# Performance work log

Hardware: AMD Instinct MI355X
Metric: run time of the kernel (lower is better)

Reference implementation:

```python
import jax, jax.numpy as jnp
import numpy as np

D = 1  # dilation


def _unfold3x3(x, d):
    # x: [B, C, H, W] -> [B, H*W, 9, C]; matches torch.nn.Unfold(kernel_size=3,
    # dilation=d, padding=d, stride=1) followed by the module's reshapes.
    B, C, H, W = x.shape
    xp = jnp.pad(x, ((0, 0), (0, 0), (d, d), (d, d)))
    pats = [xp[:, :, i * d:i * d + H, j * d:j * d + W] for i in range(3) for j in range(3)]
    p = jnp.stack(pats, axis=0)  # [9, B, C, H, W], kernel positions row-major (center = 4)
    return p.transpose(1, 3, 4, 0, 2).reshape(B, H * W, 9, C)


def _masked_bn(h, m, gamma, beta, eps=1e-5):
    # BatchNorm1d in training mode applied only to rows selected by bool mask m
    # (the torch code gathers rows, BNs them, scatters back into zeros).
    # Stats are the biased mean/var over the selected rows, per channel.
    axes = tuple(range(h.ndim - 1))
    mf = m[..., None].astype(h.dtype)
    n = jnp.maximum(mf.sum(), 1.0)
    mean = (h * mf).sum(axes) / n
    var = (((h - mean) ** 2 * mf)).sum(axes) / n
    return (h - mean) * jax.lax.rsqrt(var + eps) * gamma + beta


def setup_inputs() -> dict:
    key = jax.random.key(0)
    ks = jax.random.split(key, 8)
    B, H, W = 2, 64, 1024
    Cin, Cout, Cm = 64, 64, 4
    s = 0.1
    x = jax.random.normal(ks[0], (B, Cm + Cin, H, W), jnp.float32)
    mask = (jax.random.uniform(ks[1], (B, 1, H, W)) > 0.3).astype(jnp.float32)
    return {
        "x": x,
        "mask": mask,
        "w1": jax.random.normal(ks[2], (8, Cm), jnp.float32) * s,
        "bn1_g": jnp.ones(8, jnp.float32),
        "bn1_b": jnp.zeros(8, jnp.float32),
        "w2": jax.random.normal(ks[3], (1, 8), jnp.float32) * s,
        "b2": jnp.zeros(1, jnp.float32),
        "g1": jax.random.normal(ks[4], (8, Cm), jnp.float32) * s,
        "gbn1_g": jnp.ones(8, jnp.float32),
        "gbn1_b": jnp.zeros(8, jnp.float32),
        "g2": jax.random.normal(ks[5], (8, 8), jnp.float32) * s,
        "gbn2_g": jnp.ones(8, jnp.float32),
        "gbn2_b": jnp.zeros(8, jnp.float32),
        "w_agg": jax.random.normal(ks[6], (Cout, 72 + Cin), jnp.float32) * s,
        "abn_g": jnp.ones(Cout, jnp.float32),
        "abn_b": jnp.zeros(Cout, jnp.float32),
    }


def reference(x, mask, w1, bn1_g, bn1_b, w2, b2, g1, gbn1_g, gbn1_b, g2, gbn2_g, gbn2_b, w_agg, abn_g, abn_b):
    B, C, H, W = x.shape
    xu = _unfold3x3(x, D)                      # [B, HW, 9, C]
    mu = _unfold3x3(mask, D)[..., 0]           # [B, HW, 9]
    msel = mu > 0                              # valid-neighbor mask
    mp0 = msel[:, :, 4]                        # valid-center mask [B, HW]
    pn = xu[..., :4] - xu[:, :, 4:5, :4]       # relative meta coords [B, HW, 9, 4]
    feats = xu[..., 4:]                        # neighbor features [B, HW, 9, Cin]

    # weight branch (dense compute + mask == torch's gather/scatter)
    h = _masked_bn(pn @ w1.T, msel, bn1_g, bn1_b)
    h = jax.nn.relu(h) @ w2.T + b2             # [B, HW, 9, 1]
    wts = jnp.where(msel, h[..., 0], 0.0)      # zeros at invalid neighbors pre-softmax
    wts = jax.nn.softmax(wts, axis=-1)[..., None]

    fagg = (wts * feats).sum(axis=2)           # [B, HW, Cin]

    # geo branch
    g = jax.nn.relu(_masked_bn(pn @ g1.T, msel, gbn1_g, gbn1_b))
    g = jax.nn.relu(_masked_bn(g @ g2.T, msel, gbn2_g, gbn2_b))
    g = jnp.where(msel[..., None], g, 0.0)
    g = (wts * g).reshape(B, H * W, 72)

    # aggregation over valid centers
    out = jnp.concatenate([fagg, g], axis=-1) @ w_agg.T
    out = jax.nn.relu(_masked_bn(out, mp0, abn_g, abn_b))
    out = jnp.where(mp0[..., None], out, 0.0)  # [B, HW, Cout]
    return out.transpose(0, 2, 1).reshape(B, -1, H, W)  # fold with k=1 == reshape
```

## Files before the change

### kernel.cpp

```cpp
#include <hip/hip_runtime.h>

#define HW_ 65536
#define W_ 1024
#define H_ 64
#define B_ 2
#define C_ 68
#define NPIX 131072
#define EPS 1e-5f

typedef __attribute__((ext_vector_type(8))) short short8;
typedef __attribute__((ext_vector_type(4))) float floatx4;

__device__ __forceinline__ unsigned short f2bf(float f) {
  unsigned u = __float_as_uint(f);
  u += 0x7fffu + ((u >> 16) & 1u);
  return (unsigned short)(u >> 16);
}
__device__ __forceinline__ unsigned pack2(float a, float b) {
  return (unsigned)f2bf(a) | ((unsigned)f2bf(b) << 16);
}
__device__ __forceinline__ float wred(float v) {
  v += __shfl_xor(v, 1);  v += __shfl_xor(v, 2);  v += __shfl_xor(v, 4);
  v += __shfl_xor(v, 8);  v += __shfl_xor(v, 16); v += __shfl_xor(v, 32);
  return v;
}
__device__ __forceinline__ int swz_tile(int bid) {
  return (bid & 7) * 64 + (bid >> 3);
}

__global__ __launch_bounds__(256) void k_stats1(
    const float* __restrict__ x, const float* __restrict__ mask,
    const float* __restrict__ w1, const float* __restrict__ g1,
    float* __restrict__ ws) {
  int half = blockIdx.x >> 9;
  int p = swz_tile(blockIdx.x & 511) * 256 + threadIdx.x;
  int b = p >> 16, s = p & (HW_ - 1);
  int h = s >> 10, w = s & (W_ - 1);
  const float* xb = x + (size_t)b * C_ * HW_;
  const float* mb = mask + (size_t)b * HW_;
  float xc0 = xb[s], xc1 = xb[HW_ + s], xc2 = xb[2 * HW_ + s], xc3 = xb[3 * HW_ + s];

  float acc[34];
#pragma unroll
  for (int i = 0; i < 34; i++) acc[i] = 0.f;
  if (half == 0) acc[33] = (mb[s] > 0.f) ? 1.f : 0.f;

#pragma unroll
  for (int k = 0; k < 9; k++) {
    bool mine = (k < 5) ? (half == 0) : (half == 1);
    if (!mine) continue;
    int di = k / 3 - 1, dj = k % 3 - 1;
    int hh = h + di, ww = w + dj;
    bool inb = ((unsigned)hh < (unsigned)H_) && ((unsigned)ww < (unsigned)W_);
    int ns = hh * W_ + ww;
    float mval = inb ? mb[ns] : 0.f;
    if (mval > 0.f) {
      float pn0 = xb[ns] - xc0;
      float pn1 = xb[HW_ + ns] - xc1;
      float pn2 = xb[2 * HW_ + ns] - xc2;
      float pn3 = xb[3 * HW_ + ns] - xc3;
      acc[32] += 1.f;
#pragma unroll
      for (int o = 0; o < 8; o++) {
        float ta = pn0 * w1[o * 4] + pn1 * w1[o * 4 + 1] + pn2 * w1[o * 4 + 2] + pn3 * w1[o * 4 + 3];
        acc[o] += ta; acc[8 + o] += ta * ta;
        float tg = pn0 * g1[o * 4] + pn1 * g1[o * 4 + 1] + pn2 * g1[o * 4 + 2] + pn3 * g1[o * 4 + 3];
        acc[16 + o] += tg; acc[24 + o] += tg * tg;
      }
    }
  }
  __shared__ float red[4][34];
  int lane = threadIdx.x & 63, wave = threadIdx.x >> 6;
#pragma unroll
  for (int i = 0; i < 34; i++) {
    float rv = wred(acc[i]);
    if (lane == 0) red[wave][i] = rv;
  }
  __syncthreads();
  if (threadIdx.x < 34)
    atomicAdd(&ws[threadIdx.x],
              red[0][threadIdx.x] + red[1][threadIdx.x] + red[2][threadIdx.x] + red[3][threadIdx.x]);
}

__global__ __launch_bounds__(256) void k_stats2(
    const float* __restrict__ x, const float* __restrict__ mask,
    const float* __restrict__ g1, const float* __restrict__ gbn1_g,
    const float* __restrict__ gbn1_b, const float* __restrict__ g2,
    float* __restrict__ ws) {
  __shared__ float sc[8], sh[8];
  if (threadIdx.x < 8) {
    int o = threadIdx.x;
    float n = fmaxf(ws[32], 1.f);
    float mean = ws[16 + o] / n;
    float var = ws[24 + o] / n - mean * mean;
    float s_ = gbn1_g[o] * rsqrtf(var + EPS);
    sc[o] = s_; sh[o] = gbn1_b[o] - mean * s_;
  }
  __syncthreads();

  int half = blockIdx.x >> 9;
  int p = swz_tile(blockIdx.x & 511) * 256 + threadIdx.x;
  int b = p >> 16, s = p & (HW_ - 1);
  int h = s >> 10, w = s & (W_ - 1);
  const float* xb = x + (size_t)b * C_ * HW_;
  const float* mb = mask + (size_t)b * HW_;
  float xc0 = xb[s], xc1 = xb[HW_ + s], xc2 = xb[2 * HW_ + s], xc3 = xb[3 * HW_ + s];

  float acc2[16];
#pragma unroll
  for (int i = 0; i < 16; i++) acc2[i] = 0.f;

#pragma unroll
  for (int k = 0; k < 9; k++) {
    bool mine = (k < 5) ? (half == 0) : (half == 1);
    if (!mine) continue;
    int di = k / 3 - 1, dj = k % 3 - 1;
    int hh = h + di, ww = w + dj;
    bool inb = ((unsigned)hh < (unsigned)H_) && ((unsigned)ww < (unsigned)W_);
    int ns = hh * W_ + ww;
    float mval = inb ? mb[ns] : 0.f;
    if (mval > 0.f) {
      float pn0 = xb[ns] - xc0;
      float pn1 = xb[HW_ + ns] - xc1;
      float pn2 = xb[2 * HW_ + ns] - xc2;
      float pn3 = xb[3 * HW_ + ns] - xc3;
      float gb[8];
#pragma unroll
      for (int o = 0; o < 8; o++) {
        float tg = pn0 * g1[o * 4] + pn1 * g1[o * 4 + 1] + pn2 * g1[o * 4 + 2] + pn3 * g1[o * 4 + 3];
        gb[o] = fmaxf(sc[o] * tg + sh[o], 0.f);
      }
#pragma unroll
      for (int j = 0; j < 8; j++) {
        float t2 = 0.f;
#pragma unroll
        for (int o = 0; o < 8; o++) t2 += gb[o] * g2[j * 8 + o];
        acc2[j] += t2; acc2[8 + j] += t2 * t2;
      }
    }
  }
  __shared__ float red[4][16];
  int lane = threadIdx.x & 63, wave = threadIdx.x >> 6;
#pragma unroll
  for (int i = 0; i < 16; i++) {
    float rv = wred(acc2[i]);
    if (lane == 0) red[wave][i] = rv;
  }
  __syncthreads();
  if (threadIdx.x < 16)
    atomicAdd(&ws[40 + threadIdx.x],
              red[0][threadIdx.x] + red[1][threadIdx.x] + red[2][threadIdx.x] + red[3][threadIdx.x]);
}

__global__ __launch_bounds__(512, 4) void k_fused(
    const float* __restrict__ x, const float* __restrict__ mask,
    const float* __restrict__ w1, const float* __restrict__ bn1_g,
    const float* __restrict__ bn1_b, const float* __restrict__ w2,
    const float* __restrict__ b2, const float* __restrict__ g1,
    const float* __restrict__ gbn1_g, const float* __restrict__ gbn1_b,
    const float* __restrict__ g2, const float* __restrict__ gbn2_g,
    const float* __restrict__ gbn2_b, const float* __restrict__ w_agg,
    const float* __restrict__ ws, float* __restrict__ out_pre,
    float* __restrict__ wsum) {
  __shared__ uint4 vecA[17][256];
  __shared__ float evb[9][256];
  __shared__ float sA[8], hA[8], sG1[8], hG1[8], sG2[8], hG2[8];

  if (threadIdx.x < 24) {
    int o = threadIdx.x & 7;
    float n = fmaxf(ws[32], 1.f);
    float sum, sum2, gma, bta;
    if (threadIdx.x < 8)       { sum = ws[o];      sum2 = ws[8 + o];  gma = bn1_g[o];  bta = bn1_b[o]; }
    else if (threadIdx.x < 16) { sum = ws[16 + o]; sum2 = ws[24 + o]; gma = gbn1_g[o]; bta = gbn1_b[o]; }
    else                       { sum = ws[40 + o]; sum2 = ws[48 + o]; gma = gbn2_g[o]; bta = gbn2_b[o]; }
    float mean = sum / n, var = sum2 / n - mean * mean;
    float s_ = gma * rsqrtf(var + EPS);
    float sft = bta - mean * s_;
    if (threadIdx.x < 8)       { sA[o] = s_;  hA[o] = sft; }
    else if (threadIdx.x < 16) { sG1[o] = s_; hG1[o] = sft; }
    else                       { sG2[o] = s_; hG2[o] = sft; }
  }
  __syncthreads();

  int tid = threadIdx.x;
  int half = tid >> 8;
  int pix = tid & 255;
  int tile = swz_tile(blockIdx.x);
  int p0 = tile * 256;
  int p = p0 + pix;
  int b = p >> 16, s = p & (HW_ - 1);
  int h = s >> 10, w = s & (W_ - 1);
  const float* xb = x + (size_t)b * C_ * HW_;
  const float* mb = mask + (size_t)b * HW_;
  float xc0 = xb[s], xc1 = xb[HW_ + s], xc2 = xb[2 * HW_ + s], xc3 = xb[3 * HW_ + s];
  float b2v = b2[0];

  unsigned mbits = 0u;
#pragma unroll
  for (int k = 0; k < 9; k++) {
    bool mine = (k < 5) ? (half == 0) : (half == 1);
    if (!mine) continue;
    int di = k / 3 - 1, dj = k % 3 - 1;
    int hh = h + di, ww = w + dj;
    bool inb = ((unsigned)hh < (unsigned)H_) && ((unsigned)ww < (unsigned)W_);
    int ns = hh * W_ + ww;
    float mval = inb ? mb[ns] : 0.f;
    float wp = 0.f;
    if (mval > 0.f) {
      mbits |= (1u << k);
      float pn0 = xb[ns] - xc0;
      float pn1 = xb[HW_ + ns] - xc1;
      float pn2 = xb[2 * HW_ + ns] - xc2;
      float pn3 = xb[3 * HW_ + ns] - xc3;
      float accw = 0.f;
#pragma unroll
      for (int o = 0; o < 8; o++) {
        float ta = pn0 * w1[o * 4] + pn1 * w1[o * 4 + 1] + pn2 * w1[o * 4 + 2] + pn3 * w1[o * 4 + 3];
        accw += fmaxf(sA[o] * ta + hA[o], 0.f) * w2[o];
      }
      wp = accw + b2v;
    }
    evb[k][pix] = wp;
  }
  __syncthreads();

  float ev[9];
  float mx = -1e30f;
#pragma unroll
  for (int k = 0; k < 9; k++) { ev[k] = evb[k][pix]; mx = fmaxf(mx, ev[k]); }
  float den = 0.f;
#pragma unroll
  for (int k = 0; k < 9; k++) { ev[k] = __expf(ev[k] - mx); den += ev[k]; }
  float inv = 1.f / den;

#pragma unroll
  for (int k = 0; k < 9; k++) {
    bool mine = (k < 5) ? (half == 0) : (half == 1);
    if (!mine) continue;
    uint4 pk; pk.x = pk.y = pk.z = pk.w = 0u;
    if ((mbits >> k) & 1u) {
      int di = k / 3 - 1, dj = k % 3 - 1;
      int ns = (h + di) * W_ + (w + dj);
      float wt = ev[k] * inv;
      float pn0 = xb[ns] - xc0;
      float pn1 = xb[HW_ + ns] - xc1;
      float pn2 = xb[2 * HW_ + ns] - xc2;
      float pn3 = xb[3 * HW_ + ns] - xc3;
      float gb[8];
#pragma unroll
      for (int o = 0; o < 8; o++) {
        float tg = pn0 * g1[o * 4] + pn1 * g1[o * 4 + 1] + pn2 * g1[o * 4 + 2] + pn3 * g1[o * 4 + 3];
        gb[o] = fmaxf(sG1[o] * tg + hG1[o], 0.f);
      }
      float gv[8];
#pragma unroll
      for (int j = 0; j < 8; j++) {
        float t2 = 0.f;
#pragma unroll
        for (int o = 0; o < 8; o++) t2 += gb[o] * g2[j * 8 + o];
        float gg = fmaxf(sG2[j] * t2 + hG2[j], 0.f);
        gv[j] = wt * gg;
      }
      pk.x = pack2(gv[0], gv[1]); pk.y = pack2(gv[2], gv[3]);
      pk.z = pack2(gv[4], gv[5]); pk.w = pack2(gv[6], gv[7]);
    }
    vecA[8 + k][pix] = pk;
  }

  float facc[32];
#pragma unroll
  for (int c = 0; c < 32; c++) facc[c] = 0.f;
#pragma unroll
  for (int k = 0; k < 9; k++) {
    int di = k / 3 - 1, dj = k % 3 - 1;
    int hh = h + di, ww = w + dj;
    bool inb = ((unsigned)hh < (unsigned)H_) && ((unsigned)ww < (unsigned)W_);
    if (inb) {
      int ns = hh * W_ + ww;
      float wt = ev[k] * inv;
      const float* xf = xb + (size_t)(4 + half * 32) * HW_ + ns;
#pragma unroll
      for (int c = 0; c < 32; c++) facc[c] += wt * xf[c * HW_];
    }
  }
#pragma unroll
  for (int c0 = 0; c0 < 32; c0 += 8) {
    uint4 pk;
    pk.x = pack2(facc[c0], facc[c0 + 1]);     pk.y = pack2(facc[c0 + 2], facc[c0 + 3]);
    pk.z = pack2(facc[c0 + 4], facc[c0 + 5]); pk.w = pack2(facc[c0 + 6], facc[c0 + 7]);
    vecA[(half * 32 + c0) >> 3][pix] = pk;
  }
  __syncthreads();

  int lane = tid & 63, wave = tid >> 6;
  int q = lane >> 4, r = lane & 15;
  int wr = wave >> 1, wc = wave & 1;

  short8 Bf[2][5];
#pragma unroll
  for (int nt = 0; nt < 2; nt++) {
    int n = wc * 32 + nt * 16 + r;
#pragma unroll
    for (int ks = 0; ks < 5; ks++) {
      int k0 = ks * 32 + q * 8;
      uint4 pk; pk.x = pk.y = pk.z = pk.w = 0u;
      if (k0 < 136) {
        float4 f0 = *reinterpret_cast<const float4*>(w_agg + n * 136 + k0);
        float4 f1 = *reinterpret_cast<const float4*>(w_agg + n * 136 + k0 + 4);
        pk.x = pack2(f0.x, f0.y); pk.y = pack2(f0.z, f0.w);
        pk.z = pack2(f1.x, f1.y); pk.w = pack2(f1.z, f1.w);
      }
      Bf[nt][ks] = *reinterpret_cast<short8*>(&pk);
    }
  }

  floatx4 acc[4][2];
#pragma unroll
  for (int m = 0; m < 4; m++)
#pragma unroll
    for (int nt = 0; nt < 2; nt++) acc[m][nt] = (floatx4){0.f, 0.f, 0.f, 0.f};

#pragma unroll
  for (int m = 0; m < 4; m++) {
    int pixm = (wr * 4 + m) * 16 + r;
    short8 Af[5];
#pragma unroll
    for (int ks = 0; ks < 5; ks++) {
      int chunk = ks * 4 + q;
      if (chunk < 17)
        Af[ks] = *reinterpret_cast<const short8*>(&vecA[chunk][pixm]);
      else
        Af[ks] = (short8){0, 0, 0, 0, 0, 0, 0, 0};
    }
#pragma unroll
    for (int nt = 0; nt < 2; nt++)
#pragma unroll
      for (int ks = 0; ks < 5; ks++)
        acc[m][nt] = __builtin_amdgcn_mfma_f32_16x16x32_bf16(Af[ks], Bf[nt][ks], acc[m][nt], 0, 0, 0);
  }

  float aS[2] = {0.f, 0.f}, aQ[2] = {0.f, 0.f};
  int s0 = p0 & (HW_ - 1);
#pragma unroll
  for (int m = 0; m < 4; m++) {
    int mt = wr * 4 + m;
    int srow = s0 + mt * 16 + q * 4;
    float4 mv = *reinterpret_cast<const float4*>(mb + srow);
    float m0 = (mv.x > 0.f) ? 1.f : 0.f, m1 = (mv.y > 0.f) ? 1.f : 0.f;
    float m2 = (mv.z > 0.f) ? 1.f : 0.f, m3 = (mv.w > 0.f) ? 1.f : 0.f;
#pragma unroll
    for (int nt = 0; nt < 2; nt++) {
      int ch = wc * 32 + nt * 16 + r;
      float4 ov;
      ov.x = acc[m][nt][0]; ov.y = acc[m][nt][1];
      ov.z = acc[m][nt][2]; ov.w = acc[m][nt][3];
      aS[nt] += ov.x * m0 + ov.y * m1 + ov.z * m2 + ov.w * m3;
      aQ[nt] += ov.x * ov.x * m0 + ov.y * ov.y * m1 + ov.z * ov.z * m2 + ov.w * ov.w * m3;
      *reinterpret_cast<float4*>(out_pre + ((size_t)(b * 64 + ch)) * HW_ + srow) = ov;
    }
  }

  __syncthreads();
  float* rS = (float*)&vecA[0][0];
  float* rQ = rS + 256;
#pragma unroll
  for (int nt = 0; nt < 2; nt++) {
    float v1 = aS[nt], v2 = aQ[nt];
    v1 += __shfl_xor(v1, 16); v1 += __shfl_xor(v1, 32);
    v2 += __shfl_xor(v2, 16); v2 += __shfl_xor(v2, 32);
    if (lane < 16) { rS[wave * 32 + nt * 16 + lane] = v1; rQ[wave * 32 + nt * 16 + lane] = v2; }
  }
  __syncthreads();
  if (tid < 64) {
    int c = tid;
    int wc_ = c >> 5, nt_ = (c >> 4) & 1, r_ = c & 15;
    float s1 = 0.f, s2 = 0.f;
#pragma unroll
    for (int wr_ = 0; wr_ < 4; wr_++) {
      int idx = (wr_ * 2 + wc_) * 32 + nt_ * 16 + r_;
      s1 += rS[idx]; s2 += rQ[idx];
    }
    atomicAdd(&wsum[64 + c], s1);
    atomicAdd(&wsum[128 + c], s2);
  }
}

__global__ __launch_bounds__(256) void k_final(
    const float* __restrict__ out_pre, const float* __restrict__ mask,
    const float* __restrict__ abn_g, const float* __restrict__ abn_b,
    const float* __restrict__ ws, float* __restrict__ out) {
  __shared__ float sc[64], sh[64];
  if (threadIdx.x < 64) {
    int c = threadIdx.x;
    float n0 = fmaxf(ws[33], 1.f);
    float mean = ws[64 + c] / n0;
    float var = ws[128 + c] / n0 - mean * mean;
    float s_ = abn_g[c] * rsqrtf(var + EPS);
    sc[c] = s_; sh[c] = abn_b[c] - mean * s_;
  }
  __syncthreads();
  int i4 = (blockIdx.x * 256 + threadIdx.x) * 4;
  if (i4 >= B_ * 64 * HW_) return;
  int c = (i4 >> 16) & 63;
  int b = i4 >> 22;
  int s = i4 & (HW_ - 1);
  float4 v = *reinterpret_cast<const float4*>(out_pre + i4);
  float4 m = *reinterpret_cast<const float4*>(mask + (size_t)b * HW_ + s);
  float4 o;
  o.x = (m.x > 0.f) ? fmaxf(v.x * sc[c] + sh[c], 0.f) : 0.f;
  o.y = (m.y > 0.f) ? fmaxf(v.y * sc[c] + sh[c], 0.f) : 0.f;
  o.z = (m.z > 0.f) ? fmaxf(v.z * sc[c] + sh[c], 0.f) : 0.f;
  o.w = (m.w > 0.f) ? fmaxf(v.w * sc[c] + sh[c], 0.f) : 0.f;
  *reinterpret_cast<float4*>(out + i4) = o;
}

extern "C" void kernel_launch(void* const* d_in, const int* in_sizes, int n_in,
                              void* d_out, int out_size, void* d_ws, size_t ws_size,
                              hipStream_t stream) {
  const float* x      = (const float*)d_in[0];
  const float* mask   = (const float*)d_in[1];
  const float* w1     = (const float*)d_in[2];
  const float* bn1_g  = (const float*)d_in[3];
  const float* bn1_b  = (const float*)d_in[4];
  const float* w2     = (const float*)d_in[5];
  const float* b2     = (const float*)d_in[6];
  const float* g1     = (const float*)d_in[7];
  const float* gbn1_g = (const float*)d_in[8];
  const float* gbn1_b = (const float*)d_in[9];
  const float* g2     = (const float*)d_in[10];
  const float* gbn2_g = (const float*)d_in[11];
  const float* gbn2_b = (const float*)d_in[12];
  const float* w_agg  = (const float*)d_in[13];
  const float* abn_g  = (const float*)d_in[14];
  const float* abn_b  = (const float*)d_in[15];
  float* out = (float*)d_out;

  size_t need = 1024 + (size_t)NPIX * 64 * 4;
  if (ws_size < need) return;

  float* wsf = (float*)d_ws;
  float* out_pre = (float*)((char*)d_ws + 1024);

  hipMemsetAsync(d_ws, 0, 1024, stream);
  k_stats1<<<1024, 256, 0, stream>>>(x, mask, w1, g1, wsf);
  k_stats2<<<1024, 256, 0, stream>>>(x, mask, g1, gbn1_g, gbn1_b, g2, wsf);
  k_fused<<<512, 512, 0, stream>>>(x, mask, w1, bn1_g, bn1_b, w2, b2, g1,
                                   gbn1_g, gbn1_b, g2, gbn2_g, gbn2_b, w_agg,
                                   wsf, out_pre, wsf);
  k_final<<<8192, 256, 0, stream>>>(out_pre, mask, abn_g, abn_b, wsf, out);
}
```

Measured before the change: 208.2 us.

## Fuse final BN into main kernel via grid barrier, split stats into quarters

Removes the out_pre intermediate buffer and the separate k_final kernel. k_fused now keeps its accumulators in registers, waits at a software grid-wide barrier until all blocks have added their channel statistics, and then applies BN, ReLU and the mask before writing the output directly. This saves a 32MB write and read of the intermediate. Separately, the stats kernels split the 9 neighbors across 4 block groups instead of 2, launching 2048 blocks for more parallelism. The barrier relies on all 512 blocks being co-resident and has a spin timeout that could silently give wrong results if they are not.

```diff
diff --git a/kernel.cpp b/kernel.cpp
--- a/kernel.cpp
+++ b/kernel.cpp
@@ -6,6 +6,7 @@
 #define B_ 2
 #define C_ 68
 #define NPIX 131072
+#define NBLK_F 512
 #define EPS 1e-5f
 
 typedef __attribute__((ext_vector_type(8))) short short8;
@@ -27,12 +28,44 @@
 __device__ __forceinline__ int swz_tile(int bid) {
   return (bid & 7) * 64 + (bid >> 3);
 }
+__device__ __forceinline__ float wsld(const float* p) {
+  return __hip_atomic_load(p, __ATOMIC_RELAXED, __HIP_MEMORY_SCOPE_AGENT);
+}
+
+__device__ __forceinline__ void gridbar(unsigned* bar, unsigned nblk) {
+  __syncthreads();
+  if (threadIdx.x == 0) {
+    __threadfence();
+    unsigned gen = __hip_atomic_load(&bar[1], __ATOMIC_RELAXED, __HIP_MEMORY_SCOPE_AGENT);
+    unsigned arrived =
+        __hip_atomic_fetch_add(&bar[0], 1u, __ATOMIC_ACQ_REL, __HIP_MEMORY_SCOPE_AGENT);
+    if (arrived == nblk - 1) {
+      __hip_atomic_store(&bar[0], 0u, __ATOMIC_RELAXED, __HIP_MEMORY_SCOPE_AGENT);
+      __hip_atomic_store(&bar[1], gen + 1u, __ATOMIC_RELEASE, __HIP_MEMORY_SCOPE_AGENT);
+    } else {
+      long long spins = 0;
+      while (__hip_atomic_load(&bar[1], __ATOMIC_ACQUIRE, __HIP_MEMORY_SCOPE_AGENT) == gen) {
+        if (++spins > (1LL << 22)) break;
+        __builtin_amdgcn_s_sleep(8);
+      }
+    }
+    __threadfence();
+  }
+  __syncthreads();
+}
+
+__device__ __forceinline__ bool owns_k(int quarter, int k) {
+  return (quarter == 0) ? (k < 3)
+       : (quarter == 1) ? (k >= 3 && k < 5)
+       : (quarter == 2) ? (k >= 5 && k < 7)
+       :                  (k >= 7);
+}
 
 __global__ __launch_bounds__(256) void k_stats1(
     const float* __restrict__ x, const float* __restrict__ mask,
     const float* __restrict__ w1, const float* __restrict__ g1,
     float* __restrict__ ws) {
-  int half = blockIdx.x >> 9;
+  int quarter = blockIdx.x >> 9;
   int p = swz_tile(blockIdx.x & 511) * 256 + threadIdx.x;
   int b = p >> 16, s = p & (HW_ - 1);
   int h = s >> 10, w = s & (W_ - 1);
@@ -43,12 +76,11 @@
   float acc[34];
 #pragma unroll
   for (int i = 0; i < 34; i++) acc[i] = 0.f;
-  if (half == 0) acc[33] = (mb[s] > 0.f) ? 1.f : 0.f;
+  if (quarter == 1) acc[33] = (mb[s] > 0.f) ? 1.f : 0.f;
 
 #pragma unroll
   for (int k = 0; k < 9; k++) {
-    bool mine = (k < 5) ? (half == 0) : (half == 1);
-    if (!mine) continue;
+    if (!owns_k(quarter, k)) continue;
     int di = k / 3 - 1, dj = k % 3 - 1;
     int hh = h + di, ww = w + dj;
     bool inb = ((unsigned)hh < (unsigned)H_) && ((unsigned)ww < (unsigned)W_);
@@ -98,7 +130,7 @@
   }
   __syncthreads();
 
-  int half = blockIdx.x >> 9;
+  int quarter = blockIdx.x >> 9;
   int p = swz_tile(blockIdx.x & 511) * 256 + threadIdx.x;
   int b = p >> 16, s = p & (HW_ - 1);
   int h = s >> 10, w = s & (W_ - 1);
@@ -112,8 +144,7 @@
 
 #pragma unroll
   for (int k = 0; k < 9; k++) {
-    bool mine = (k < 5) ? (half == 0) : (half == 1);
-    if (!mine) continue;
+    if (!owns_k(quarter, k)) continue;
     int di = k / 3 - 1, dj = k % 3 - 1;
     int hh = h + di, ww = w + dj;
     bool inb = ((unsigned)hh < (unsigned)H_) && ((unsigned)ww < (unsigned)W_);
@@ -160,11 +191,13 @@
     const float* __restrict__ gbn1_g, const float* __restrict__ gbn1_b,
     const float* __restrict__ g2, const float* __restrict__ gbn2_g,
     const float* __restrict__ gbn2_b, const float* __restrict__ w_agg,
-    const float* __restrict__ ws, float* __restrict__ out_pre,
-    float* __restrict__ wsum) {
+    const float* __restrict__ abn_g, const float* __restrict__ abn_b,
+    float* __restrict__ ws, float* __restrict__ out) {
+  unsigned* bar = (unsigned*)(ws + 248);
   __shared__ uint4 vecA[17][256];
   __shared__ float evb[9][256];
   __shared__ float sA[8], hA[8], sG1[8], hG1[8], sG2[8], hG2[8];
+  __shared__ float scD[64], shD[64];
 
   if (threadIdx.x < 24) {
     int o = threadIdx.x & 7;
@@ -350,13 +383,9 @@
     float m2 = (mv.z > 0.f) ? 1.f : 0.f, m3 = (mv.w > 0.f) ? 1.f : 0.f;
 #pragma unroll
     for (int nt = 0; nt < 2; nt++) {
-      int ch = wc * 32 + nt * 16 + r;
-      float4 ov;
-      ov.x = acc[m][nt][0]; ov.y = acc[m][nt][1];
-      ov.z = acc[m][nt][2]; ov.w = acc[m][nt][3];
-      aS[nt] += ov.x * m0 + ov.y * m1 + ov.z * m2 + ov.w * m3;
-      aQ[nt] += ov.x * ov.x * m0 + ov.y * ov.y * m1 + ov.z * ov.z * m2 + ov.w * ov.w * m3;
-      *reinterpret_cast<float4*>(out_pre + ((size_t)(b * 64 + ch)) * HW_ + srow) = ov;
+      aS[nt] += acc[m][nt][0] * m0 + acc[m][nt][1] * m1 + acc[m][nt][2] * m2 + acc[m][nt][3] * m3;
+      aQ[nt] += acc[m][nt][0] * acc[m][nt][0] * m0 + acc[m][nt][1] * acc[m][nt][1] * m1 +
+                acc[m][nt][2] * acc[m][nt][2] * m2 + acc[m][nt][3] * acc[m][nt][3] * m3;
     }
   }
 
@@ -380,38 +409,38 @@
       int idx = (wr_ * 2 + wc_) * 32 + nt_ * 16 + r_;
       s1 += rS[idx]; s2 += rQ[idx];
     }
-    atomicAdd(&wsum[64 + c], s1);
-    atomicAdd(&wsum[128 + c], s2);
-  }
-}
-
-__global__ __launch_bounds__(256) void k_final(
-    const float* __restrict__ out_pre, const float* __restrict__ mask,
-    const float* __restrict__ abn_g, const float* __restrict__ abn_b,
-    const float* __restrict__ ws, float* __restrict__ out) {
-  __shared__ float sc[64], sh[64];
-  if (threadIdx.x < 64) {
-    int c = threadIdx.x;
-    float n0 = fmaxf(ws[33], 1.f);
-    float mean = ws[64 + c] / n0;
-    float var = ws[128 + c] / n0 - mean * mean;
+    atomicAdd(&ws[64 + c], s1);
+    atomicAdd(&ws[128 + c], s2);
+  }
+
+  gridbar(bar, NBLK_F);
+
+  if (tid < 64) {
+    int c = tid;
+    float n0 = fmaxf(wsld(&ws[33]), 1.f);
+    float mean = wsld(&ws[64 + c]) / n0;
+    float var = wsld(&ws[128 + c]) / n0 - mean * mean;
     float s_ = abn_g[c] * rsqrtf(var + EPS);
-    sc[c] = s_; sh[c] = abn_b[c] - mean * s_;
-  }
-  __syncthreads();
-  int i4 = (blockIdx.x * 256 + threadIdx.x) * 4;
-  if (i4 >= B_ * 64 * HW_) return;
-  int c = (i4 >> 16) & 63;
-  int b = i4 >> 22;
-  int s = i4 & (HW_ - 1);
-  float4 v = *reinterpret_cast<const float4*>(out_pre + i4);
-  float4 m = *reinterpret_cast<const float4*>(mask + (size_t)b * HW_ + s);
-  float4 o;
-  o.x = (m.x > 0.f) ? fmaxf(v.x * sc[c] + sh[c], 0.f) : 0.f;
-  o.y = (m.y > 0.f) ? fmaxf(v.y * sc[c] + sh[c], 0.f) : 0.f;
-  o.z = (m.z > 0.f) ? fmaxf(v.z * sc[c] + sh[c], 0.f) : 0.f;
-  o.w = (m.w > 0.f) ? fmaxf(v.w * sc[c] + sh[c], 0.f) : 0.f;
-  *reinterpret_cast<float4*>(out + i4) = o;
+    scD[c] = s_; shD[c] = abn_b[c] - mean * s_;
+  }
+  __syncthreads();
+#pragma unroll
+  for (int m = 0; m < 4; m++) {
+    int mt = wr * 4 + m;
+    int srow = s0 + mt * 16 + q * 4;
+    float4 mv = *reinterpret_cast<const float4*>(mb + srow);
+#pragma unroll
+    for (int nt = 0; nt < 2; nt++) {
+      int ch = wc * 32 + nt * 16 + r;
+      float sc_ = scD[ch], sh_ = shD[ch];
+      float4 ov;
+      ov.x = (mv.x > 0.f) ? fmaxf(acc[m][nt][0] * sc_ + sh_, 0.f) : 0.f;
+      ov.y = (mv.y > 0.f) ? fmaxf(acc[m][nt][1] * sc_ + sh_, 0.f) : 0.f;
+      ov.z = (mv.z > 0.f) ? fmaxf(acc[m][nt][2] * sc_ + sh_, 0.f) : 0.f;
+      ov.w = (mv.w > 0.f) ? fmaxf(acc[m][nt][3] * sc_ + sh_, 0.f) : 0.f;
+      *reinterpret_cast<float4*>(out + ((size_t)(b * 64 + ch)) * HW_ + srow) = ov;
+    }
+  }
 }
 
 extern "C" void kernel_launch(void* const* d_in, const int* in_sizes, int n_in,
@@ -435,17 +464,13 @@
   const float* abn_b  = (const float*)d_in[15];
   float* out = (float*)d_out;
 
-  size_t need = 1024 + (size_t)NPIX * 64 * 4;
-  if (ws_size < need) return;
-
+  if (ws_size < 1024) return;
   float* wsf = (float*)d_ws;
-  float* out_pre = (float*)((char*)d_ws + 1024);
 
   hipMemsetAsync(d_ws, 0, 1024, stream);
-  k_stats1<<<1024, 256, 0, stream>>>(x, mask, w1, g1, wsf);
-  k_stats2<<<1024, 256, 0, stream>>>(x, mask, g1, gbn1_g, gbn1_b, g2, wsf);
-  k_fused<<<512, 512, 0, stream>>>(x, mask, w1, bn1_g, bn1_b, w2, b2, g1,
-                                   gbn1_g, gbn1_b, g2, gbn2_g, gbn2_b, w_agg,
-                                   wsf, out_pre, wsf);
-  k_final<<<8192, 256, 0, stream>>>(out_pre, mask, abn_g, abn_b, wsf, out);
-}
+  k_stats1<<<2048, 256, 0, stream>>>(x, mask, w1, g1, wsf);
+  k_stats2<<<2048, 256, 0, stream>>>(x, mask, g1, gbn1_g, gbn1_b, g2, wsf);
+  k_fused<<<NBLK_F, 512, 0, stream>>>(x, mask, w1, bn1_g, bn1_b, w2, b2, g1,
+                                      gbn1_g, gbn1_b, g2, gbn2_g, gbn2_b, w_agg,
+                                      abn_g, abn_b, wsf, out);
+}
```

Measured after the change: 377.6 us. +81.3%, slower.

## Stage 3-row halo of meta channels and mask in LDS for stencil kernels

Applied to the files above, without the earlier changes.

Each block now cooperatively loads the three rows (with one-column halo) of the four meta channels and the mask into shared memory, and the stencil neighbor reads in both stats kernels and the fused kernel come from LDS instead of repeated global loads. In the fused kernel the staging buffer aliases the vecA operand buffer. The relative coordinates are cached in registers so the geo branch no longer reloads them. This cuts redundant global and cache traffic at the cost of extra LDS, a block-wide barrier before compute, and more register pressure.

```diff
diff --git a/kernel.cpp b/kernel.cpp
--- a/kernel.cpp
+++ b/kernel.cpp
@@ -7,6 +7,8 @@
 #define C_ 68
 #define NPIX 131072
 #define EPS 1e-5f
+#define SCOLS 258
+#define STOT (15 * SCOLS)
 
 typedef __attribute__((ext_vector_type(8))) short short8;
 typedef __attribute__((ext_vector_type(4))) float floatx4;
@@ -28,37 +30,61 @@
   return (bid & 7) * 64 + (bid >> 3);
 }
 
-__global__ __launch_bounds__(256) void k_stats1(
+#define XSTG(ch, row, col) stg[((ch) * 3 + (row)) * SCOLS + (col)]
+#define MSTG(row, col)     stg[(12 + (row)) * SCOLS + (col)]
+
+template <int NT>
+__device__ __forceinline__ void stage_rows(const float* xb, const float* mb,
+                                           int h, int w0, float* stg, int tid) {
+#pragma unroll 1
+  for (int i = tid; i < STOT; i += NT) {
+    int seg = i / SCOLS, col = i - seg * SCOLS;
+    int arr = seg / 3, row = seg - arr * 3;
+    int wg = w0 - 1 + col, hg = h + row - 1;
+    bool ok = ((unsigned)wg < (unsigned)W_) && ((unsigned)hg < (unsigned)H_);
+    float v = 0.f;
+    if (ok) v = (arr < 4) ? xb[(size_t)arr * HW_ + (hg << 10) + wg]
+                          : mb[(hg << 10) + wg];
+    stg[i] = v;
+  }
+}
+
+__global__ __launch_bounds__(256, 4) void k_stats1(
     const float* __restrict__ x, const float* __restrict__ mask,
     const float* __restrict__ w1, const float* __restrict__ g1,
     float* __restrict__ ws) {
+  __shared__ float stg[STOT];
+  __shared__ float red[4][34];
   int half = blockIdx.x >> 9;
-  int p = swz_tile(blockIdx.x & 511) * 256 + threadIdx.x;
-  int b = p >> 16, s = p & (HW_ - 1);
-  int h = s >> 10, w = s & (W_ - 1);
+  int tile = swz_tile(blockIdx.x & 511);
+  int p0 = tile * 256;
+  int b = p0 >> 16, s0 = p0 & (HW_ - 1);
+  int h = s0 >> 10, w0 = s0 & (W_ - 1);
   const float* xb = x + (size_t)b * C_ * HW_;
   const float* mb = mask + (size_t)b * HW_;
-  float xc0 = xb[s], xc1 = xb[HW_ + s], xc2 = xb[2 * HW_ + s], xc3 = xb[3 * HW_ + s];
+  stage_rows<256>(xb, mb, h, w0, stg, threadIdx.x);
+  __syncthreads();
+
+  int pix = threadIdx.x;
+  float xc0 = XSTG(0, 1, 1 + pix), xc1 = XSTG(1, 1, 1 + pix);
+  float xc2 = XSTG(2, 1, 1 + pix), xc3 = XSTG(3, 1, 1 + pix);
 
   float acc[34];
 #pragma unroll
   for (int i = 0; i < 34; i++) acc[i] = 0.f;
-  if (half == 0) acc[33] = (mb[s] > 0.f) ? 1.f : 0.f;
-
+  if (half == 0) acc[33] = (MSTG(1, 1 + pix) > 0.f) ? 1.f : 0.f;
+
+  int kb = half ? 5 : 0, ke = half ? 9 : 5;
 #pragma unroll
   for (int k = 0; k < 9; k++) {
-    bool mine = (k < 5) ? (half == 0) : (half == 1);
-    if (!mine) continue;
-    int di = k / 3 - 1, dj = k % 3 - 1;
-    int hh = h + di, ww = w + dj;
-    bool inb = ((unsigned)hh < (unsigned)H_) && ((unsigned)ww < (unsigned)W_);
-    int ns = hh * W_ + ww;
-    float mval = inb ? mb[ns] : 0.f;
+    if (k < kb || k >= ke) continue;
+    int row = k / 3, col = 1 + pix + (k % 3 - 1);
+    float mval = MSTG(row, col);
     if (mval > 0.f) {
-      float pn0 = xb[ns] - xc0;
-      float pn1 = xb[HW_ + ns] - xc1;
-      float pn2 = xb[2 * HW_ + ns] - xc2;
-      float pn3 = xb[3 * HW_ + ns] - xc3;
+      float pn0 = XSTG(0, row, col) - xc0;
+      float pn1 = XSTG(1, row, col) - xc1;
+      float pn2 = XSTG(2, row, col) - xc2;
+      float pn3 = XSTG(3, row, col) - xc3;
       acc[32] += 1.f;
 #pragma unroll
       for (int o = 0; o < 8; o++) {
@@ -69,7 +95,6 @@
       }
     }
   }
-  __shared__ float red[4][34];
   int lane = threadIdx.x & 63, wave = threadIdx.x >> 6;
 #pragma unroll
   for (int i = 0; i < 34; i++) {
@@ -82,11 +107,13 @@
               red[0][threadIdx.x] + red[1][threadIdx.x] + red[2][threadIdx.x] + red[3][threadIdx.x]);
 }
 
-__global__ __launch_bounds__(256) void k_stats2(
+__global__ __launch_bounds__(256, 4) void k_stats2(
     const float* __restrict__ x, const float* __restrict__ mask,
     const float* __restrict__ g1, const float* __restrict__ gbn1_g,
     const float* __restrict__ gbn1_b, const float* __restrict__ g2,
     float* __restrict__ ws) {
+  __shared__ float stg[STOT];
+  __shared__ float red[4][16];
   __shared__ float sc[8], sh[8];
   if (threadIdx.x < 8) {
     int o = threadIdx.x;
@@ -96,34 +123,35 @@
     float s_ = gbn1_g[o] * rsqrtf(var + EPS);
     sc[o] = s_; sh[o] = gbn1_b[o] - mean * s_;
   }
-  __syncthreads();
-
   int half = blockIdx.x >> 9;
-  int p = swz_tile(blockIdx.x & 511) * 256 + threadIdx.x;
-  int b = p >> 16, s = p & (HW_ - 1);
-  int h = s >> 10, w = s & (W_ - 1);
+  int tile = swz_tile(blockIdx.x & 511);
+  int p0 = tile * 256;
+  int b = p0 >> 16, s0 = p0 & (HW_ - 1);
+  int h = s0 >> 10, w0 = s0 & (W_ - 1);
   const float* xb = x + (size_t)b * C_ * HW_;
   const float* mb = mask + (size_t)b * HW_;
-  float xc0 = xb[s], xc1 = xb[HW_ + s], xc2 = xb[2 * HW_ + s], xc3 = xb[3 * HW_ + s];
+  stage_rows<256>(xb, mb, h, w0, stg, threadIdx.x);
+  __syncthreads();
+
+  int pix = threadIdx.x;
+  float xc0 = XSTG(0, 1, 1 + pix), xc1 = XSTG(1, 1, 1 + pix);
+  float xc2 = XSTG(2, 1, 1 + pix), xc3 = XSTG(3, 1, 1 + pix);
 
   float acc2[16];
 #pragma unroll
   for (int i = 0; i < 16; i++) acc2[i] = 0.f;
 
+  int kb = half ? 5 : 0, ke = half ? 9 : 5;
 #pragma unroll
   for (int k = 0; k < 9; k++) {
-    bool mine = (k < 5) ? (half == 0) : (half == 1);
-    if (!mine) continue;
-    int di = k / 3 - 1, dj = k % 3 - 1;
-    int hh = h + di, ww = w + dj;
-    bool inb = ((unsigned)hh < (unsigned)H_) && ((unsigned)ww < (unsigned)W_);
-    int ns = hh * W_ + ww;
-    float mval = inb ? mb[ns] : 0.f;
+    if (k < kb || k >= ke) continue;
+    int row = k / 3, col = 1 + pix + (k % 3 - 1);
+    float mval = MSTG(row, col);
     if (mval > 0.f) {
-      float pn0 = xb[ns] - xc0;
-      float pn1 = xb[HW_ + ns] - xc1;
-      float pn2 = xb[2 * HW_ + ns] - xc2;
-      float pn3 = xb[3 * HW_ + ns] - xc3;
+      float pn0 = XSTG(0, row, col) - xc0;
+      float pn1 = XSTG(1, row, col) - xc1;
+      float pn2 = XSTG(2, row, col) - xc2;
+      float pn3 = XSTG(3, row, col) - xc3;
       float gb[8];
 #pragma unroll
       for (int o = 0; o < 8; o++) {
@@ -139,7 +167,6 @@
       }
     }
   }
-  __shared__ float red[4][16];
   int lane = threadIdx.x & 63, wave = threadIdx.x >> 6;
 #pragma unroll
   for (int i = 0; i < 16; i++) {
@@ -165,6 +192,7 @@
   __shared__ uint4 vecA[17][256];
   __shared__ float evb[9][256];
   __shared__ float sA[8], hA[8], sG1[8], hG1[8], sG2[8], hG2[8];
+  float* stg = (float*)&vecA[0][0];
 
   if (threadIdx.x < 24) {
     int o = threadIdx.x & 7;
@@ -180,42 +208,45 @@
     else if (threadIdx.x < 16) { sG1[o] = s_; hG1[o] = sft; }
     else                       { sG2[o] = s_; hG2[o] = sft; }
   }
-  __syncthreads();
 
   int tid = threadIdx.x;
   int half = tid >> 8;
   int pix = tid & 255;
   int tile = swz_tile(blockIdx.x);
   int p0 = tile * 256;
-  int p = p0 + pix;
-  int b = p >> 16, s = p & (HW_ - 1);
-  int h = s >> 10, w = s & (W_ - 1);
+  int b = p0 >> 16, s0 = p0 & (HW_ - 1);
+  int h = s0 >> 10, w0 = s0 & (W_ - 1);
   const float* xb = x + (size_t)b * C_ * HW_;
   const float* mb = mask + (size_t)b * HW_;
-  float xc0 = xb[s], xc1 = xb[HW_ + s], xc2 = xb[2 * HW_ + s], xc3 = xb[3 * HW_ + s];
+  stage_rows<512>(xb, mb, h, w0, stg, tid);
+  __syncthreads();
+
+  float xc0 = XSTG(0, 1, 1 + pix), xc1 = XSTG(1, 1, 1 + pix);
+  float xc2 = XSTG(2, 1, 1 + pix), xc3 = XSTG(3, 1, 1 + pix);
   float b2v = b2[0];
 
+  float pnc[5][4];
   unsigned mbits = 0u;
+  int kb = half ? 5 : 0, ke = half ? 9 : 5;
 #pragma unroll
   for (int k = 0; k < 9; k++) {
-    bool mine = (k < 5) ? (half == 0) : (half == 1);
-    if (!mine) continue;
-    int di = k / 3 - 1, dj = k % 3 - 1;
-    int hh = h + di, ww = w + dj;
-    bool inb = ((unsigned)hh < (unsigned)H_) && ((unsigned)ww < (unsigned)W_);
-    int ns = hh * W_ + ww;
-    float mval = inb ? mb[ns] : 0.f;
+    if (k < kb || k >= ke) continue;
+    int j = k - kb;
+    int row = k / 3, col = 1 + pix + (k % 3 - 1);
+    float mval = MSTG(row, col);
     float wp = 0.f;
+    pnc[j][0] = 0.f; pnc[j][1] = 0.f; pnc[j][2] = 0.f; pnc[j][3] = 0.f;
     if (mval > 0.f) {
       mbits |= (1u << k);
-      float pn0 = xb[ns] - xc0;
-      float pn1 = xb[HW_ + ns] - xc1;
-      float pn2 = xb[2 * HW_ + ns] - xc2;
-      float pn3 = xb[3 * HW_ + ns] - xc3;
+      pnc[j][0] = XSTG(0, row, col) - xc0;
+      pnc[j][1] = XSTG(1, row, col) - xc1;
+      pnc[j][2] = XSTG(2, row, col) - xc2;
+      pnc[j][3] = XSTG(3, row, col) - xc3;
       float accw = 0.f;
 #pragma unroll
       for (int o = 0; o < 8; o++) {
-        float ta = pn0 * w1[o * 4] + pn1 * w1[o * 4 + 1] + pn2 * w1[o * 4 + 2] + pn3 * w1[o * 4 + 3];
+        float ta = pnc[j][0] * w1[o * 4] + pnc[j][1] * w1[o * 4 + 1] +
+                   pnc[j][2] * w1[o * 4 + 2] + pnc[j][3] * w1[o * 4 + 3];
         accw += fmaxf(sA[o] * ta + hA[o], 0.f) * w2[o];
       }
       wp = accw + b2v;
@@ -235,31 +266,26 @@
 
 #pragma unroll
   for (int k = 0; k < 9; k++) {
-    bool mine = (k < 5) ? (half == 0) : (half == 1);
-    if (!mine) continue;
+    if (k < kb || k >= ke) continue;
+    int j = k - kb;
     uint4 pk; pk.x = pk.y = pk.z = pk.w = 0u;
     if ((mbits >> k) & 1u) {
-      int di = k / 3 - 1, dj = k % 3 - 1;
-      int ns = (h + di) * W_ + (w + dj);
       float wt = ev[k] * inv;
-      float pn0 = xb[ns] - xc0;
-      float pn1 = xb[HW_ + ns] - xc1;
-      float pn2 = xb[2 * HW_ + ns] - xc2;
-      float pn3 = xb[3 * HW_ + ns] - xc3;
       float gb[8];
 #pragma unroll
       for (int o = 0; o < 8; o++) {
-        float tg = pn0 * g1[o * 4] + pn1 * g1[o * 4 + 1] + pn2 * g1[o * 4 + 2] + pn3 * g1[o * 4 + 3];
+        float tg = pnc[j][0] * g1[o * 4] + pnc[j][1] * g1[o * 4 + 1] +
+                   pnc[j][2] * g1[o * 4 + 2] + pnc[j][3] * g1[o * 4 + 3];
         gb[o] = fmaxf(sG1[o] * tg + hG1[o], 0.f);
       }
       float gv[8];
 #pragma unroll
-      for (int j = 0; j < 8; j++) {
+      for (int j2 = 0; j2 < 8; j2++) {
         float t2 = 0.f;
 #pragma unroll
-        for (int o = 0; o < 8; o++) t2 += gb[o] * g2[j * 8 + o];
-        float gg = fmaxf(sG2[j] * t2 + hG2[j], 0.f);
-        gv[j] = wt * gg;
+        for (int o = 0; o < 8; o++) t2 += gb[o] * g2[j2 * 8 + o];
+        float gg = fmaxf(sG2[j2] * t2 + hG2[j2], 0.f);
+        gv[j2] = wt * gg;
       }
       pk.x = pack2(gv[0], gv[1]); pk.y = pack2(gv[2], gv[3]);
       pk.z = pack2(gv[4], gv[5]); pk.w = pack2(gv[6], gv[7]);
@@ -273,14 +299,14 @@
 #pragma unroll
   for (int k = 0; k < 9; k++) {
     int di = k / 3 - 1, dj = k % 3 - 1;
-    int hh = h + di, ww = w + dj;
+    int hh = h + di, ww = w0 + pix + dj;
     bool inb = ((unsigned)hh < (unsigned)H_) && ((unsigned)ww < (unsigned)W_);
     if (inb) {
-      int ns = hh * W_ + ww;
+      int ns = (hh << 10) + ww;
       float wt = ev[k] * inv;
       const float* xf = xb + (size_t)(4 + half * 32) * HW_ + ns;
 #pragma unroll
-      for (int c = 0; c < 32; c++) facc[c] += wt * xf[c * HW_];
+      for (int c = 0; c < 32; c++) facc[c] += wt * xf[(size_t)c * HW_];
     }
   }
 #pragma unroll
@@ -340,7 +366,6 @@
   }
 
   float aS[2] = {0.f, 0.f}, aQ[2] = {0.f, 0.f};
-  int s0 = p0 & (HW_ - 1);
 #pragma unroll
   for (int m = 0; m < 4; m++) {
     int mt = wr * 4 + m;
```

New measurement: 209.9 us. Within noise of the previous version (+0.8%).
